# Performance work log

Hardware: AMD Instinct MI355X
Metric: run time of the kernel (lower is better)

## Reference

```python
import jax, jax.numpy as jnp
import numpy as np

B, S, E, H, R = 2, 2048, 1024, 16, 8
D = E // H  # head depth = 64


def setup_inputs() -> dict:
    key = jax.random.key(0)
    ks = jax.random.split(key, 16)
    sd = 1.0 / np.sqrt(E)
    inp = {
        'q': jax.random.normal(ks[0], (B, S, E), jnp.float32),
        'k': jax.random.normal(ks[1], (B, S, E), jnp.float32),
        'v': jax.random.normal(ks[2], (B, S, E), jnp.float32),
        # Q projection (Dense + LoRA)
        'wq': jax.random.normal(ks[3], (E, E), jnp.float32) * sd,
        'bq': jnp.zeros((E,), jnp.float32),
        'wq_a': jax.random.normal(ks[4], (E, R), jnp.float32) * sd,
        'wq_b': jax.random.normal(ks[5], (R, E), jnp.float32) * 0.01,
        # K projection (plain Dense)
        'wk': jax.random.normal(ks[6], (E, E), jnp.float32) * sd,
        'bk': jnp.zeros((E,), jnp.float32),
        # V projection (Dense + LoRA)
        'wv': jax.random.normal(ks[7], (E, E), jnp.float32) * sd,
        'bv': jnp.zeros((E,), jnp.float32),
        'wv_a': jax.random.normal(ks[8], (E, R), jnp.float32) * sd,
        'wv_b': jax.random.normal(ks[9], (R, E), jnp.float32) * 0.01,
        # output projection
        'wo': jax.random.normal(ks[10], (E, E), jnp.float32) * sd,
        'bo': jnp.zeros((E,), jnp.float32),
    }
    return inp


def _lora_dense(x, w, b, w_a, w_b):
    # Dense(x) + (x @ A) @ B
    return x @ w + b + (x @ w_a) @ w_b


def _split_heads(x):
    # [B,S,E] -> [B,H,S,D]
    return x.reshape(B, S, H, D).transpose(0, 2, 1, 3)


def reference(q, k, v, wq, bq, wq_a, wq_b, wk, bk, wv, bv, wv_a, wv_b, wo, bo):
    qh = _split_heads(_lora_dense(q, wq, bq, wq_a, wq_b))
    kh = _split_heads(k @ wk + bk)
    vh = _split_heads(_lora_dense(v, wv, bv, wv_a, wv_b))
    # scaled dot-product attention per head
    scale = 1.0 / jnp.sqrt(jnp.asarray(D, jnp.float32))
    logits = jnp.einsum('bhqd,bhkd->bhqk', qh, kh) * scale
    attn = jax.nn.softmax(logits, axis=-1)
    out = jnp.einsum('bhqk,bhkd->bhqd', attn, vh)  # [B,H,S,D]
    out = out.transpose(0, 2, 1, 3).reshape(B, S, E)
    return out @ wo + bo
```

## Files before the change

### kernel.cpp

```cpp
#include <hip/hip_runtime.h>

typedef __attribute__((ext_vector_type(8))) _Float16 f16x8;
typedef __attribute__((ext_vector_type(4))) _Float16 f16x4;
typedef __attribute__((ext_vector_type(4))) float f32x4;

static __device__ __forceinline__ f16x4 pack4(float a, float b, float c, float d) {
    f16x4 r;
    auto p0 = __builtin_amdgcn_cvt_pkrtz(a, b);
    auto p1 = __builtin_amdgcn_cvt_pkrtz(c, d);
    r[0] = p0[0]; r[1] = p0[1]; r[2] = p1[0]; r[3] = p1[1];
    return r;
}

static __device__ __forceinline__ f16x8 cvt8(float4 u0, float4 u1) {
    f16x8 r;
    auto p = __builtin_amdgcn_cvt_pkrtz(u0.x, u0.y); r[0] = p[0]; r[1] = p[1];
    p = __builtin_amdgcn_cvt_pkrtz(u0.z, u0.w);      r[2] = p[0]; r[3] = p[1];
    p = __builtin_amdgcn_cvt_pkrtz(u1.x, u1.y);      r[4] = p[0]; r[5] = p[1];
    p = __builtin_amdgcn_cvt_pkrtz(u1.z, u1.w);      r[6] = p[0]; r[7] = p[1];
    return r;
}

static __device__ __forceinline__ void gll16(const void* g, void* l) {
    __builtin_amdgcn_global_load_lds(
        (const __attribute__((address_space(1))) unsigned int*)g,
        (__attribute__((address_space(3))) unsigned int*)l, 16, 0, 0);
}

__global__ __launch_bounds__(256) void tsplit_w16(const float* __restrict__ w0, const float* __restrict__ w1,
                                                  const float* __restrict__ w2, const float* __restrict__ w3,
                                                  _Float16* __restrict__ th) {
    const float* W = blockIdx.z == 0 ? w0 : blockIdx.z == 1 ? w1 : blockIdx.z == 2 ? w2 : w3;
    _Float16* oh = th + (size_t)blockIdx.z * 1048576;
    __shared__ float t[64][65];
    const int tid = threadIdx.x;
    const int kt = blockIdx.x, nb = blockIdx.y;
    const int k0 = kt * 64, n0 = nb * 64;
    const int c = tid & 15, r = tid >> 4;
#pragma unroll
    for (int i = 0; i < 4; ++i) {
        const int row = r + i * 16;
        const float4 v4 = *(const float4*)&W[(size_t)(k0 + row) * 1024 + n0 + c * 4];
        t[c * 4 + 0][row] = v4.x;
        t[c * 4 + 1][row] = v4.y;
        t[c * 4 + 2][row] = v4.z;
        t[c * 4 + 3][row] = v4.w;
    }
    __syncthreads();
    const size_t tb = (size_t)(nb * 16 + kt) * 4096;
#pragma unroll
    for (int i = 0; i < 2; ++i) {
        const int cid = tid * 2 + i;
        const int rr = cid >> 3, cc = cid & 7;
        const int ksrc = (cc ^ (rr & 7)) * 8;
        f16x8 hv;
#pragma unroll
        for (int j = 0; j < 8; ++j) hv[j] = (_Float16)t[rr][ksrc + j];
        *(f16x8*)&oh[tb + cid * 8] = hv;
    }
}

__global__ __launch_bounds__(256) void prep_lora(const float* __restrict__ q, const float* __restrict__ kk,
                                                 const float* __restrict__ v,
                                                 const float* __restrict__ wqa, const float* __restrict__ wva,
                                                 float* __restrict__ xaq, float* __restrict__ xav,
                                                 _Float16* __restrict__ o16) {
    const int y = blockIdx.y;
    const float* X = y == 0 ? q : y == 1 ? v : kk;
    _Float16* O = o16 + (size_t)(y == 0 ? 0 : y == 1 ? 2 : 1) * 4194304;
    const float* WA = y == 0 ? wqa : wva;
    float* XA = y == 0 ? xaq : xav;
    const int tid = threadIdx.x;
    const int w = tid >> 6, lane = tid & 63;
    const int m = blockIdx.x * 4 + w;
    const float* xrow = X + (size_t)m * 1024;
    _Float16* orow = O + (size_t)m * 1024;
    float s[8] = {};
#pragma unroll
    for (int i = 0; i < 4; ++i) {
        const int k = lane * 4 + i * 256;
        const float4 x4 = *(const float4*)&xrow[k];
        *(f16x4*)&orow[k] = pack4(x4.x, x4.y, x4.z, x4.w);
        if (y < 2) {
            const float xs[4] = {x4.x, x4.y, x4.z, x4.w};
#pragma unroll
            for (int j = 0; j < 4; ++j) {
                const float* wr = WA + (size_t)(k + j) * 8;
                const float xv = xs[j];
#pragma unroll
                for (int rr = 0; rr < 8; ++rr) s[rr] = fmaf(xv, wr[rr], s[rr]);
            }
        }
    }
    if (y < 2) {
#pragma unroll
        for (int rr = 0; rr < 8; ++rr) {
            float vv = s[rr];
            vv += __shfl_xor(vv, 32);
            vv += __shfl_xor(vv, 16);
            vv += __shfl_xor(vv, 8);
            vv += __shfl_xor(vv, 4);
            vv += __shfl_xor(vv, 2);
            vv += __shfl_xor(vv, 1);
            if (lane == 0) XA[(size_t)m * 8 + rr] = vv;
        }
    }
}

template <int OUT, bool LORA>
__global__ __launch_bounds__(256) void gemm_v3(const _Float16* __restrict__ A,
                                               const _Float16* __restrict__ Bt,
                                               const float* __restrict__ bias,
                                               const float* __restrict__ XA,
                                               const float* __restrict__ WB,
                                               float scale,
                                               void* __restrict__ outp) {
    __shared__ _Float16 Ahs[2][4096], Bhs[2][4096];
    const int tid = threadIdx.x;
    const int w = tid >> 6, l = tid & 63;
    const int lm = l & 15, g = l >> 4;
    const int wm = w >> 1, wn = w & 1;
    const int m0 = blockIdx.x * 64, nb = blockIdx.y, n0 = nb * 64;

    const int lr = l >> 3;
    const int ksw = ((l & 7) ^ lr) * 8;
    const _Float16* Asrc0 = A + (size_t)(m0 + w * 16 + lr) * 1024 + ksw;
    const _Float16* Asrc1 = A + (size_t)(m0 + w * 16 + 8 + lr) * 1024 + ksw;
    const _Float16* Bsrc0 = Bt + (size_t)nb * 65536 + (w * 128 + l) * 8;
    const _Float16* Bsrc1 = Bt + (size_t)nb * 65536 + (w * 128 + 64 + l) * 8;
    const int adst0 = w * 1024, adst1 = w * 1024 + 512;

    int afo[2][2], bfo[2][2];
#pragma unroll
    for (int t = 0; t < 2; ++t)
#pragma unroll
        for (int kc = 0; kc < 2; ++kc) {
            const int ar = wm * 32 + t * 16 + lm;
            const int br = wn * 32 + t * 16 + lm;
            afo[t][kc] = ar * 64 + (((kc * 4 + g) ^ (ar & 7)) * 8);
            bfo[t][kc] = br * 64 + (((kc * 4 + g) ^ (br & 7)) * 8);
        }

    f32x4 acc[2][2] = {};

#define STAGE(buf, kt)                                  \
    {                                                   \
        const int ko = (kt) * 64;                       \
        const int bo = (kt) * 4096;                     \
        gll16(Asrc0 + ko, &Ahs[buf][adst0]);            \
        gll16(Asrc1 + ko, &Ahs[buf][adst1]);            \
        gll16(Bsrc0 + bo, &Bhs[buf][adst0]);            \
        gll16(Bsrc1 + bo, &Bhs[buf][adst1]);            \
    }

    STAGE(0, 0)
    __syncthreads();

    for (int kt = 0; kt < 16; ++kt) {
        const int cur = kt & 1;
        if (kt < 15) STAGE(cur ^ 1, kt + 1)
        const _Float16* Ac = &Ahs[cur][0];
        const _Float16* Bc = &Bhs[cur][0];
#pragma unroll
        for (int kc = 0; kc < 2; ++kc) {
            f16x8 ah[2], bh[2];
#pragma unroll
            for (int i = 0; i < 2; ++i) {
                ah[i] = *(const f16x8*)&Ac[afo[i][kc]];
                bh[i] = *(const f16x8*)&Bc[bfo[i][kc]];
            }
            __builtin_amdgcn_s_setprio(1);
#pragma unroll
            for (int mt = 0; mt < 2; ++mt)
#pragma unroll
                for (int nt = 0; nt < 2; ++nt)
                    acc[mt][nt] = __builtin_amdgcn_mfma_f32_16x16x32_f16(ah[mt], bh[nt], acc[mt][nt], 0, 0, 0);
            __builtin_amdgcn_s_setprio(0);
        }
        __syncthreads();
    }
#undef STAGE

    const int nbase = n0 + wn * 32;
    const int head = nb;
    float bias2[2];
#pragma unroll
    for (int nt = 0; nt < 2; ++nt) bias2[nt] = bias[nbase + nt * 16 + lm];
    float wbv[8][2];
    if (LORA) {
#pragma unroll
        for (int rr = 0; rr < 8; ++rr)
#pragma unroll
            for (int nt = 0; nt < 2; ++nt) wbv[rr][nt] = WB[rr * 1024 + nbase + nt * 16 + lm];
    }
#pragma unroll
    for (int mt = 0; mt < 2; ++mt) {
        float ov[2][4];
#pragma unroll
        for (int r = 0; r < 4; ++r) {
            const int m = m0 + wm * 32 + mt * 16 + g * 4 + r;
            float xa8[8];
            if (LORA) {
#pragma unroll
                for (int rr = 0; rr < 8; ++rr) xa8[rr] = XA[(size_t)m * 8 + rr];
            }
#pragma unroll
            for (int nt = 0; nt < 2; ++nt) {
                float o = acc[mt][nt][r] + bias2[nt];
                if (LORA) {
#pragma unroll
                    for (int rr = 0; rr < 8; ++rr) o = fmaf(xa8[rr], wbv[rr][nt], o);
                }
                o *= scale;
                ov[nt][r] = o;
                if (OUT == 0) {
                    ((float*)outp)[(size_t)m * 1024 + nbase + nt * 16 + lm] = o;
                } else if (OUT == 1) {
                    const int b = m >> 11, s = m & 2047;
                    ((_Float16*)outp)[((size_t)(b * 16 + head) * 2048 + s) * 64 + wn * 32 + nt * 16 + lm] = (_Float16)o;
                }
            }
        }
        if (OUT == 2) {
            const int b = m0 >> 11;
            const int sb = (m0 & 2047) + wm * 32 + mt * 16 + g * 4;
#pragma unroll
            for (int nt = 0; nt < 2; ++nt) {
                const int d = wn * 32 + nt * 16 + lm;
                const f16x4 pv = pack4(ov[nt][0], ov[nt][1], ov[nt][2], ov[nt][3]);
                *(f16x4*)&((_Float16*)outp)[((size_t)(b * 16 + head) * 64 + d) * 2048 + sb] = pv;
            }
        }
    }
}

__global__ __launch_bounds__(256, 2) void flash_attn9(const _Float16* __restrict__ qh,
                                                      const _Float16* __restrict__ kh,
                                                      const _Float16* __restrict__ vT,
                                                      _Float16* __restrict__ ao) {
    __shared__ _Float16 Ks[2][4096];
    __shared__ _Float16 Vs[2][4096];
    const int tid = threadIdx.x;
    const int w = tid >> 6, l = tid & 63;
    const int m = l & 15, g = l >> 4;
    const int bh = blockIdx.x & 31, qt = blockIdx.x >> 5;
    const _Float16* Qb = qh + (size_t)bh * 131072;
    const _Float16* Kb = kh + (size_t)bh * 131072;
    const _Float16* Vb = vT + (size_t)bh * 131072;
    const int q0 = qt * 128 + w * 32;

    f16x8 qf[2][2];
#pragma unroll
    for (int qg = 0; qg < 2; ++qg) {
        const _Float16* qrow = Qb + (size_t)(q0 + qg * 16 + m) * 64 + g * 8;
        qf[qg][0] = *(const f16x8*)(qrow);
        qf[qg][1] = *(const f16x8*)(qrow + 32);
    }

    const int r0 = tid >> 3, c0 = tid & 7;
    const int r1 = (tid + 256) >> 3;
    const int kgl0 = r0 * 64 + c0 * 8;
    const int kgl1 = r1 * 64 + c0 * 8;
    const int kso0 = r0 * 64 + ((c0 ^ (r0 & 7)) * 8);
    const int kso1 = r1 * 64 + ((c0 ^ (r1 & 7)) * 8);
    const size_t vgl0 = (size_t)r0 * 2048 + c0 * 8;
    const size_t vgl1 = (size_t)r1 * 2048 + c0 * 8;

    int koff[4][2];
#pragma unroll
    for (int nt = 0; nt < 4; ++nt)
#pragma unroll
        for (int kc = 0; kc < 2; ++kc) {
            const int kv = nt * 16 + m;
            koff[nt][kc] = kv * 64 + (((kc * 4 + g) ^ (kv & 7)) * 8);
        }
    int voff[4][4];
#pragma unroll
    for (int dt = 0; dt < 4; ++dt)
#pragma unroll
        for (int nt = 0; nt < 4; ++nt) {
            const int d = dt * 16 + m;
            voff[dt][nt] = d * 64 + (((nt * 2 + (g >> 1)) ^ (d & 7)) * 8) + (g & 1) * 4;
        }

    f32x4 acc_o[2][4] = {};
    f32x4 acc_l[2] = {};
    const f16x4 onesf = {(_Float16)1.f, (_Float16)1.f, (_Float16)1.f, (_Float16)1.f};

    {
        const f16x8 ka = *(const f16x8*)(Kb + kgl0);
        const f16x8 kb2 = *(const f16x8*)(Kb + kgl1);
        const f16x8 va = *(const f16x8*)(Vb + vgl0);
        const f16x8 vb2 = *(const f16x8*)(Vb + vgl1);
        *(f16x8*)(&Ks[0][0] + kso0) = ka;
        *(f16x8*)(&Ks[0][0] + kso1) = kb2;
        *(f16x8*)(&Vs[0][0] + kso0) = va;
        *(f16x8*)(&Vs[0][0] + kso1) = vb2;
    }
    __syncthreads();

    for (int t = 0; t < 32; ++t) {
        const int cur = t & 1;
        f16x8 ka, kb2, va, vb2;
        if (t < 31) {
            const int koI = (t + 1) * 4096;
            const int voI = (t + 1) * 64;
            ka = *(const f16x8*)(Kb + koI + kgl0);
            kb2 = *(const f16x8*)(Kb + koI + kgl1);
            va = *(const f16x8*)(Vb + voI + vgl0);
            vb2 = *(const f16x8*)(Vb + voI + vgl1);
        }

        const _Float16* Kc = &Ks[cur][0];
        const _Float16* Vc = &Vs[cur][0];

        f32x4 s[2][4] = {};
        __builtin_amdgcn_s_setprio(1);
#pragma unroll
        for (int nt = 0; nt < 4; ++nt)
#pragma unroll
            for (int kc = 0; kc < 2; ++kc) {
                const f16x8 kf = *(const f16x8*)(Kc + koff[nt][kc]);
                s[0][nt] = __builtin_amdgcn_mfma_f32_16x16x32_f16(kf, qf[0][kc], s[0][nt], 0, 0, 0);
                s[1][nt] = __builtin_amdgcn_mfma_f32_16x16x32_f16(kf, qf[1][kc], s[1][nt], 0, 0, 0);
            }
        __builtin_amdgcn_s_setprio(0);

        f16x4 pf[2][4];
#pragma unroll
        for (int qg = 0; qg < 2; ++qg)
#pragma unroll
            for (int nt = 0; nt < 4; ++nt)
                pf[qg][nt] = pack4(exp2f(s[qg][nt][0]), exp2f(s[qg][nt][1]),
                                   exp2f(s[qg][nt][2]), exp2f(s[qg][nt][3]));

        __builtin_amdgcn_s_setprio(1);
#pragma unroll
        for (int nt = 0; nt < 4; ++nt) {
            acc_l[0] = __builtin_amdgcn_mfma_f32_16x16x16f16(onesf, pf[0][nt], acc_l[0], 0, 0, 0);
            acc_l[1] = __builtin_amdgcn_mfma_f32_16x16x16f16(onesf, pf[1][nt], acc_l[1], 0, 0, 0);
#pragma unroll
            for (int dt = 0; dt < 4; ++dt) {
                const f16x4 vf = *(const f16x4*)(Vc + voff[dt][nt]);
                acc_o[0][dt] = __builtin_amdgcn_mfma_f32_16x16x16f16(vf, pf[0][nt], acc_o[0][dt], 0, 0, 0);
                acc_o[1][dt] = __builtin_amdgcn_mfma_f32_16x16x16f16(vf, pf[1][nt], acc_o[1][dt], 0, 0, 0);
            }
        }
        __builtin_amdgcn_s_setprio(0);

        if (t < 31) {
            const int nxt = cur ^ 1;
            *(f16x8*)(&Ks[nxt][0] + kso0) = ka;
            *(f16x8*)(&Ks[nxt][0] + kso1) = kb2;
            *(f16x8*)(&Vs[nxt][0] + kso0) = va;
            *(f16x8*)(&Vs[nxt][0] + kso1) = vb2;
        }
        __syncthreads();
    }

    const int b = bh >> 4, h = bh & 15;
#pragma unroll
    for (int qg = 0; qg < 2; ++qg) {
        const float inv = 1.f / acc_l[qg][0];
        const int srow = q0 + qg * 16 + m;
        _Float16* orow = ao + ((size_t)(b * 2048 + srow)) * 1024 + h * 64;
#pragma unroll
        for (int dt = 0; dt < 4; ++dt) {
            const f16x4 o = pack4(acc_o[qg][dt][0] * inv, acc_o[qg][dt][1] * inv,
                                  acc_o[qg][dt][2] * inv, acc_o[qg][dt][3] * inv);
            *(f16x4*)&orow[dt * 16 + g * 4] = o;
        }
    }
}

extern "C" void kernel_launch(void* const* d_in, const int* in_sizes, int n_in,
                              void* d_out, int out_size, void* d_ws, size_t ws_size,
                              hipStream_t stream) {
    const float* q    = (const float*)d_in[0];
    const float* k    = (const float*)d_in[1];
    const float* v    = (const float*)d_in[2];
    const float* wq   = (const float*)d_in[3];
    const float* bq   = (const float*)d_in[4];
    const float* wq_a = (const float*)d_in[5];
    const float* wq_b = (const float*)d_in[6];
    const float* wk   = (const float*)d_in[7];
    const float* bk   = (const float*)d_in[8];
    const float* wv   = (const float*)d_in[9];
    const float* bv   = (const float*)d_in[10];
    const float* wv_a = (const float*)d_in[11];
    const float* wv_b = (const float*)d_in[12];
    const float* wo   = (const float*)d_in[13];
    const float* bo   = (const float*)d_in[14];
    float* out = (float*)d_out;

    char* wsb = (char*)d_ws;
    _Float16* Wt   = (_Float16*)(wsb);
    _Float16* a16  = (_Float16*)(wsb + (8u << 20));
    _Float16* aoF  = a16;
    _Float16* qhF  = (_Float16*)(wsb + (32u << 20));
    _Float16* khF  = (_Float16*)(wsb + (40u << 20));
    _Float16* vTF  = (_Float16*)(wsb + (48u << 20));
    float* xaq     = (float*)(wsb + (56u << 20));
    float* xav     = (float*)(wsb + (56u << 20) + (128u << 10));

    const dim3 ggrid(64, 16);
    const float qscale = 0.18033688f;

    tsplit_w16<<<dim3(16, 16, 4), 256, 0, stream>>>(wq, wk, wv, wo, Wt);
    prep_lora<<<dim3(1024, 3), 256, 0, stream>>>(q, k, v, wq_a, wv_a, xaq, xav, a16);

    gemm_v3<1, true><<<ggrid, 256, 0, stream>>>(a16, Wt, bq, xaq, wq_b, qscale, qhF);
    gemm_v3<1, false><<<ggrid, 256, 0, stream>>>(a16 + 4194304, Wt + 1048576, bk, nullptr, nullptr, 1.f, khF);
    gemm_v3<2, true><<<ggrid, 256, 0, stream>>>(a16 + 8388608, Wt + 2097152, bv, xav, wv_b, 1.f, vTF);

    flash_attn9<<<512, 256, 0, stream>>>(qhF, khF, vTF, aoF);

    gemm_v3<0, false><<<ggrid, 256, 0, stream>>>(aoF, Wt + 3145728, bo, nullptr, nullptr, 1.f, out);
}
```

Baseline: 163.7 us.

## Enlarge GEMM M-tile to 128 and stage attention K/V via direct-to-LDS loads

The projection GEMMs now compute 128x64 tiles per block, with each warp holding 4x2 MFMA accumulators. This doubles the reuse of each B tile, halves the grid to 512 blocks, and raises register and LDS use. The flash attention kernel replaces its register-staged K/V prefetch (global load, then LDS store after compute) with global_load_lds async copies into the swizzled double buffer. That removes register pressure and the explicit LDS stores. The smaller GEMM grid may underfill the 256 CUs.

```diff
diff --git a/kernel.cpp b/kernel.cpp
--- a/kernel.cpp
+++ b/kernel.cpp
@@ -9,15 +9,6 @@
     auto p0 = __builtin_amdgcn_cvt_pkrtz(a, b);
     auto p1 = __builtin_amdgcn_cvt_pkrtz(c, d);
     r[0] = p0[0]; r[1] = p0[1]; r[2] = p1[0]; r[3] = p1[1];
-    return r;
-}
-
-static __device__ __forceinline__ f16x8 cvt8(float4 u0, float4 u1) {
-    f16x8 r;
-    auto p = __builtin_amdgcn_cvt_pkrtz(u0.x, u0.y); r[0] = p[0]; r[1] = p[1];
-    p = __builtin_amdgcn_cvt_pkrtz(u0.z, u0.w);      r[2] = p[0]; r[3] = p[1];
-    p = __builtin_amdgcn_cvt_pkrtz(u1.x, u1.y);      r[4] = p[0]; r[5] = p[1];
-    p = __builtin_amdgcn_cvt_pkrtz(u1.z, u1.w);      r[6] = p[0]; r[7] = p[1];
     return r;
 }
 
@@ -108,49 +99,57 @@
 }
 
 template <int OUT, bool LORA>
-__global__ __launch_bounds__(256) void gemm_v3(const _Float16* __restrict__ A,
+__global__ __launch_bounds__(256) void gemm_v6(const _Float16* __restrict__ A,
                                                const _Float16* __restrict__ Bt,
                                                const float* __restrict__ bias,
                                                const float* __restrict__ XA,
                                                const float* __restrict__ WB,
                                                float scale,
                                                void* __restrict__ outp) {
-    __shared__ _Float16 Ahs[2][4096], Bhs[2][4096];
+    __shared__ _Float16 Ahs[2][8192];
+    __shared__ _Float16 Bhs[2][4096];
     const int tid = threadIdx.x;
     const int w = tid >> 6, l = tid & 63;
     const int lm = l & 15, g = l >> 4;
     const int wm = w >> 1, wn = w & 1;
-    const int m0 = blockIdx.x * 64, nb = blockIdx.y, n0 = nb * 64;
+    const int m0 = blockIdx.x * 128, nb = blockIdx.y;
 
     const int lr = l >> 3;
     const int ksw = ((l & 7) ^ lr) * 8;
-    const _Float16* Asrc0 = A + (size_t)(m0 + w * 16 + lr) * 1024 + ksw;
-    const _Float16* Asrc1 = A + (size_t)(m0 + w * 16 + 8 + lr) * 1024 + ksw;
-    const _Float16* Bsrc0 = Bt + (size_t)nb * 65536 + (w * 128 + l) * 8;
-    const _Float16* Bsrc1 = Bt + (size_t)nb * 65536 + (w * 128 + 64 + l) * 8;
-    const int adst0 = w * 1024, adst1 = w * 1024 + 512;
-
-    int afo[2][2], bfo[2][2];
-#pragma unroll
-    for (int t = 0; t < 2; ++t)
+    const _Float16* Asrc[4];
+#pragma unroll
+    for (int j = 0; j < 4; ++j) Asrc[j] = A + (size_t)(m0 + j * 32 + w * 8 + lr) * 1024 + ksw;
+    const _Float16* Bsrc0 = Bt + (size_t)nb * 65536 + (w * 64 + l) * 8;
+    const _Float16* Bsrc1 = Bt + (size_t)nb * 65536 + (256 + w * 64 + l) * 8;
+    const int ad[4] = {w * 512, 2048 + w * 512, 4096 + w * 512, 6144 + w * 512};
+    const int bd0 = w * 512, bd1 = 2048 + w * 512;
+
+    int afo[4][2], bfo[2][2];
+#pragma unroll
+    for (int mt = 0; mt < 4; ++mt)
 #pragma unroll
         for (int kc = 0; kc < 2; ++kc) {
-            const int ar = wm * 32 + t * 16 + lm;
-            const int br = wn * 32 + t * 16 + lm;
-            afo[t][kc] = ar * 64 + (((kc * 4 + g) ^ (ar & 7)) * 8);
-            bfo[t][kc] = br * 64 + (((kc * 4 + g) ^ (br & 7)) * 8);
-        }
-
-    f32x4 acc[2][2] = {};
-
-#define STAGE(buf, kt)                                  \
-    {                                                   \
-        const int ko = (kt) * 64;                       \
-        const int bo = (kt) * 4096;                     \
-        gll16(Asrc0 + ko, &Ahs[buf][adst0]);            \
-        gll16(Asrc1 + ko, &Ahs[buf][adst1]);            \
-        gll16(Bsrc0 + bo, &Bhs[buf][adst0]);            \
-        gll16(Bsrc1 + bo, &Bhs[buf][adst1]);            \
+            const int ar = wm * 64 + mt * 16 + lm;
+            afo[mt][kc] = ar * 64 + (((kc * 4 + g) ^ (ar & 7)) * 8);
+        }
+#pragma unroll
+    for (int nt = 0; nt < 2; ++nt)
+#pragma unroll
+        for (int kc = 0; kc < 2; ++kc) {
+            const int br = wn * 32 + nt * 16 + lm;
+            bfo[nt][kc] = br * 64 + (((kc * 4 + g) ^ (br & 7)) * 8);
+        }
+
+    f32x4 acc[4][2] = {};
+
+#define STAGE(buf, kt)                                       \
+    {                                                        \
+        const int ko = (kt) * 64;                            \
+        const int bo = (kt) * 4096;                          \
+        _Pragma("unroll") for (int j = 0; j < 4; ++j)        \
+            gll16(Asrc[j] + ko, &Ahs[buf][ad[j]]);           \
+        gll16(Bsrc0 + bo, &Bhs[buf][bd0]);                   \
+        gll16(Bsrc1 + bo, &Bhs[buf][bd1]);                   \
     }
 
     STAGE(0, 0)
@@ -163,15 +162,14 @@
         const _Float16* Bc = &Bhs[cur][0];
 #pragma unroll
         for (int kc = 0; kc < 2; ++kc) {
-            f16x8 ah[2], bh[2];
-#pragma unroll
-            for (int i = 0; i < 2; ++i) {
-                ah[i] = *(const f16x8*)&Ac[afo[i][kc]];
-                bh[i] = *(const f16x8*)&Bc[bfo[i][kc]];
-            }
+            f16x8 ah[4], bh[2];
+#pragma unroll
+            for (int i = 0; i < 4; ++i) ah[i] = *(const f16x8*)&Ac[afo[i][kc]];
+#pragma unroll
+            for (int i = 0; i < 2; ++i) bh[i] = *(const f16x8*)&Bc[bfo[i][kc]];
             __builtin_amdgcn_s_setprio(1);
 #pragma unroll
-            for (int mt = 0; mt < 2; ++mt)
+            for (int mt = 0; mt < 4; ++mt)
 #pragma unroll
                 for (int nt = 0; nt < 2; ++nt)
                     acc[mt][nt] = __builtin_amdgcn_mfma_f32_16x16x32_f16(ah[mt], bh[nt], acc[mt][nt], 0, 0, 0);
@@ -181,7 +179,7 @@
     }
 #undef STAGE
 
-    const int nbase = n0 + wn * 32;
+    const int nbase = nb * 64 + wn * 32;
     const int head = nb;
     float bias2[2];
 #pragma unroll
@@ -194,11 +192,11 @@
             for (int nt = 0; nt < 2; ++nt) wbv[rr][nt] = WB[rr * 1024 + nbase + nt * 16 + lm];
     }
 #pragma unroll
-    for (int mt = 0; mt < 2; ++mt) {
+    for (int mt = 0; mt < 4; ++mt) {
         float ov[2][4];
 #pragma unroll
         for (int r = 0; r < 4; ++r) {
-            const int m = m0 + wm * 32 + mt * 16 + g * 4 + r;
+            const int m = m0 + wm * 64 + mt * 16 + g * 4 + r;
             float xa8[8];
             if (LORA) {
 #pragma unroll
@@ -223,7 +221,7 @@
         }
         if (OUT == 2) {
             const int b = m0 >> 11;
-            const int sb = (m0 & 2047) + wm * 32 + mt * 16 + g * 4;
+            const int sb = (m0 & 2047) + wm * 64 + mt * 16 + g * 4;
 #pragma unroll
             for (int nt = 0; nt < 2; ++nt) {
                 const int d = wn * 32 + nt * 16 + lm;
@@ -234,10 +232,10 @@
     }
 }
 
-__global__ __launch_bounds__(256, 2) void flash_attn9(const _Float16* __restrict__ qh,
-                                                      const _Float16* __restrict__ kh,
-                                                      const _Float16* __restrict__ vT,
-                                                      _Float16* __restrict__ ao) {
+__global__ __launch_bounds__(256, 2) void flash_attn10(const _Float16* __restrict__ qh,
+                                                       const _Float16* __restrict__ kh,
+                                                       const _Float16* __restrict__ vT,
+                                                       _Float16* __restrict__ ao) {
     __shared__ _Float16 Ks[2][4096];
     __shared__ _Float16 Vs[2][4096];
     const int tid = threadIdx.x;
@@ -257,14 +255,22 @@
         qf[qg][1] = *(const f16x8*)(qrow + 32);
     }
 
-    const int r0 = tid >> 3, c0 = tid & 7;
-    const int r1 = (tid + 256) >> 3;
-    const int kgl0 = r0 * 64 + c0 * 8;
-    const int kgl1 = r1 * 64 + c0 * 8;
-    const int kso0 = r0 * 64 + ((c0 ^ (r0 & 7)) * 8);
-    const int kso1 = r1 * 64 + ((c0 ^ (r1 & 7)) * 8);
-    const size_t vgl0 = (size_t)r0 * 2048 + c0 * 8;
-    const size_t vgl1 = (size_t)r1 * 2048 + c0 * 8;
+    const int lr = l >> 3;
+    const int ksw = ((l & 7) ^ lr) * 8;
+    const _Float16* Ksrc0 = Kb + (size_t)(w * 8 + lr) * 64 + ksw;
+    const _Float16* Ksrc1 = Kb + (size_t)(32 + w * 8 + lr) * 64 + ksw;
+    const _Float16* Vsrc0 = Vb + (size_t)(w * 8 + lr) * 2048 + ksw;
+    const _Float16* Vsrc1 = Vb + (size_t)(32 + w * 8 + lr) * 2048 + ksw;
+    const int dst0 = w * 512, dst1 = 2048 + w * 512;
+
+#define ASTG(buf, t)                                   \
+    {                                                  \
+        const int ko = (t) * 4096, vo = (t) * 64;      \
+        gll16(Ksrc0 + ko, &Ks[buf][dst0]);             \
+        gll16(Ksrc1 + ko, &Ks[buf][dst1]);             \
+        gll16(Vsrc0 + vo, &Vs[buf][dst0]);             \
+        gll16(Vsrc1 + vo, &Vs[buf][dst1]);             \
+    }
 
     int koff[4][2];
 #pragma unroll
@@ -287,29 +293,12 @@
     f32x4 acc_l[2] = {};
     const f16x4 onesf = {(_Float16)1.f, (_Float16)1.f, (_Float16)1.f, (_Float16)1.f};
 
-    {
-        const f16x8 ka = *(const f16x8*)(Kb + kgl0);
-        const f16x8 kb2 = *(const f16x8*)(Kb + kgl1);
-        const f16x8 va = *(const f16x8*)(Vb + vgl0);
-        const f16x8 vb2 = *(const f16x8*)(Vb + vgl1);
-        *(f16x8*)(&Ks[0][0] + kso0) = ka;
-        *(f16x8*)(&Ks[0][0] + kso1) = kb2;
-        *(f16x8*)(&Vs[0][0] + kso0) = va;
-        *(f16x8*)(&Vs[0][0] + kso1) = vb2;
-    }
+    ASTG(0, 0)
     __syncthreads();
 
     for (int t = 0; t < 32; ++t) {
         const int cur = t & 1;
-        f16x8 ka, kb2, va, vb2;
-        if (t < 31) {
-            const int koI = (t + 1) * 4096;
-            const int voI = (t + 1) * 64;
-            ka = *(const f16x8*)(Kb + koI + kgl0);
-            kb2 = *(const f16x8*)(Kb + koI + kgl1);
-            va = *(const f16x8*)(Vb + voI + vgl0);
-            vb2 = *(const f16x8*)(Vb + voI + vgl1);
-        }
+        if (t < 31) ASTG(cur ^ 1, t + 1)
 
         const _Float16* Kc = &Ks[cur][0];
         const _Float16* Vc = &Vs[cur][0];
@@ -348,15 +337,9 @@
         }
         __builtin_amdgcn_s_setprio(0);
 
-        if (t < 31) {
-            const int nxt = cur ^ 1;
-            *(f16x8*)(&Ks[nxt][0] + kso0) = ka;
-            *(f16x8*)(&Ks[nxt][0] + kso1) = kb2;
-            *(f16x8*)(&Vs[nxt][0] + kso0) = va;
-            *(f16x8*)(&Vs[nxt][0] + kso1) = vb2;
-        }
         __syncthreads();
     }
+#undef ASTG
 
     const int b = bh >> 4, h = bh & 15;
 #pragma unroll
@@ -403,17 +386,17 @@
     float* xaq     = (float*)(wsb + (56u << 20));
     float* xav     = (float*)(wsb + (56u << 20) + (128u << 10));
 
-    const dim3 ggrid(64, 16);
+    const dim3 ggrid(32, 16);
     const float qscale = 0.18033688f;
 
     tsplit_w16<<<dim3(16, 16, 4), 256, 0, stream>>>(wq, wk, wv, wo, Wt);
     prep_lora<<<dim3(1024, 3), 256, 0, stream>>>(q, k, v, wq_a, wv_a, xaq, xav, a16);
 
-    gemm_v3<1, true><<<ggrid, 256, 0, stream>>>(a16, Wt, bq, xaq, wq_b, qscale, qhF);
-    gemm_v3<1, false><<<ggrid, 256, 0, stream>>>(a16 + 4194304, Wt + 1048576, bk, nullptr, nullptr, 1.f, khF);
-    gemm_v3<2, true><<<ggrid, 256, 0, stream>>>(a16 + 8388608, Wt + 2097152, bv, xav, wv_b, 1.f, vTF);
-
-    flash_attn9<<<512, 256, 0, stream>>>(qhF, khF, vTF, aoF);
-
-    gemm_v3<0, false><<<ggrid, 256, 0, stream>>>(aoF, Wt + 3145728, bo, nullptr, nullptr, 1.f, out);
-}
+    gemm_v6<1, true><<<ggrid, 256, 0, stream>>>(a16, Wt, bq, xaq, wq_b, qscale, qhF);
+    gemm_v6<1, false><<<ggrid, 256, 0, stream>>>(a16 + 4194304, Wt + 1048576, bk, nullptr, nullptr, 1.f, khF);
+    gemm_v6<2, true><<<ggrid, 256, 0, stream>>>(a16 + 8388608, Wt + 2097152, bv, xav, wv_b, 1.f, vTF);
+
+    flash_attn10<<<512, 256, 0, stream>>>(qhF, khF, vTF, aoF);
+
+    gemm_v6<0, false><<<ggrid, 256, 0, stream>>>(aoF, Wt + 3145728, bo, nullptr, nullptr, 1.f, out);
+}
```

Measured after the change: 179.5 us. 1.1x slower.
